# Optimization experiments

Hardware: AMD Instinct MI355X
Metric: run time of the kernel (lower is better)

## Reference

```python
import jax, jax.numpy as jnp
import numpy as np
from jax import lax

TOP_K = 8

B, S, D, N, R = 32, 128, 512, 131072, 16


def setup_inputs() -> dict:
    key = jax.random.key(0)
    ks = jax.random.split(key, 10)
    return {
        "query": jax.random.normal(ks[0], (B, S, D), jnp.float32),
        "base_memory": jax.random.normal(ks[1], (N, D), jnp.float32) * 0.01,
        "lora_A": jax.random.normal(ks[2], (N, R), jnp.float32) * 0.01,
        "lora_B": jax.random.normal(ks[3], (R, D), jnp.float32) * 0.01,
        "gru_w_ih": jax.random.normal(ks[4], (3 * D, D), jnp.float32) * 0.02,
        "gru_w_hh": jax.random.normal(ks[5], (3 * D, D), jnp.float32) * 0.02,
        "gru_b_ih": jax.random.normal(ks[6], (3 * D,), jnp.float32) * 0.02,
        "gru_b_hh": jax.random.normal(ks[7], (3 * D,), jnpp.float32) if False else jax.random.normal(ks[7], (3 * D,), jnp.float32) * 0.02,
        "wg_w": jax.random.normal(ks[8], (1, D), jnp.float32) * 0.02,
        "wg_b": jnp.zeros((1,), jnp.float32),
    }


def gru_cell(x, h, w_ih, w_hh, b_ih, b_hh):
    # torch.nn.GRUCell math; gates ordered [r, z, n]
    gx = x @ w_ih.T + b_ih            # [B, 3D]
    gh = h @ w_hh.T + b_hh            # [B, 3D]
    gx_r, gx_z, gx_n = jnp.split(gx, 3, axis=-1)
    gh_r, gh_z, gh_n = jnp.split(gh, 3, axis=-1)
    r = jax.nn.sigmoid(gx_r + gh_r)
    z = jax.nn.sigmoid(gx_z + gh_z)
    n = jnp.tanh(gx_n + r * gh_n)
    return (1.0 - z) * n + z * h


def reference(query, base_memory, lora_A, lora_B, gru_w_ih, gru_w_hh, gru_b_ih, gru_b_hh, wg_w, wg_b):
    mem = base_memory + lora_A @ lora_B                 # [N, D]
    q = query.mean(axis=1)                              # [B, D]
    scores = q @ mem.T                                  # [B, N]
    top_scores, top_idx = lax.top_k(scores, TOP_K)      # [B, K]
    retrieved = mem[top_idx]                            # [B, K, D] gather

    h0 = jnp.zeros_like(q)
    hidden = gru_cell(retrieved.sum(axis=1), h0, gru_w_ih, gru_w_hh, gru_b_ih, gru_b_hh)

    write_prob = jax.nn.sigmoid(hidden @ wg_w.T + wg_b)  # [B, 1]
    value = q                                            # value[b, 0] in torch == q[b]

    # Sequential over batch (matches torch loop order); within a batch the
    # top-k indices are distinct so a vectorized scatter-set is exact.
    def step(m, inp):
        idx, p, v = inp                                  # [K], scalar, [D]
        rows = (1.0 - p) * m[idx] + p * v
        return m.at[idx].set(rows), None

    new_mem, _ = lax.scan(step, base_memory, (top_idx, write_prob[:, 0], value))
    return retrieved, hidden, new_mem
```

## Files before the change

### kernel.cpp

```cpp
#include <hip/hip_runtime.h>
#include <math.h>

#define NROWS 131072
#define DDIM  512
#define BB    32
#define SS    128
#define KK    8

__global__ __launch_bounds__(256) void k_qmean(const float* __restrict__ query,
                                               float* __restrict__ q,
                                               float* __restrict__ pwsum) {
  __shared__ float part[256];
  int b  = blockIdx.x >> 3;
  int dc = blockIdx.x & 7;
  int t  = threadIdx.x;
  if (blockIdx.x == 0 && t < 32) pwsum[t] = 0.f;
  int lane = t & 63;
  int p    = t >> 6;
  const float* src = query + (size_t)b * SS * DDIM + (size_t)(p * 32) * DDIM
                   + dc * 64 + lane;
  float s = 0.f;
  #pragma unroll 8
  for (int i = 0; i < 32; ++i) s += src[(size_t)i * DDIM];
  part[t] = s;
  __syncthreads();
  if (t < 64) {
    float tot = part[t] + part[64 + t] + part[128 + t] + part[192 + t];
    q[b * DDIM + dc * 64 + t] = tot * (1.0f / 128.0f);
  }
}

__global__ __launch_bounds__(256) void k_mem(const float* __restrict__ base,
                                             const float* __restrict__ A,
                                             const float* __restrict__ Bm,
                                             float* __restrict__ newmem) {
  int gt = blockIdx.x * 256 + threadIdx.x;
  int c = gt & 127;
  int stream = gt >> 7;
  int row0 = stream * 64;
  int srow0 = __builtin_amdgcn_readfirstlane(row0);

  float4 Breg[16];
  #pragma unroll
  for (int r = 0; r < 16; ++r)
    Breg[r] = *(const float4*)(Bm + r * DDIM + 4 * c);

  const float* bp = base   + (size_t)row0 * DDIM + 4 * c;
  float*       np = newmem + (size_t)row0 * DDIM + 4 * c;

  float4 nxt0 = *(const float4*)(bp);
  float4 nxt1 = *(const float4*)(bp + DDIM);
  float4 nxt2 = *(const float4*)(bp + 2 * DDIM);
  float4 nxt3 = *(const float4*)(bp + 3 * DDIM);

  for (int i = 0; i < 64; i += 4) {
    float4 cur0 = nxt0, cur1 = nxt1, cur2 = nxt2, cur3 = nxt3;
    if (i + 4 < 64) {
      const float* p = bp + (size_t)(i + 4) * DDIM;
      nxt0 = *(const float4*)(p);
      nxt1 = *(const float4*)(p + DDIM);
      nxt2 = *(const float4*)(p + 2 * DDIM);
      nxt3 = *(const float4*)(p + 3 * DDIM);
    }
    #pragma unroll
    for (int k = 0; k < 4; ++k) {
      const float* Ar = A + (size_t)(srow0 + i + k) * 16;
      float4 acc = (k == 0) ? cur0 : (k == 1) ? cur1 : (k == 2) ? cur2 : cur3;
      #pragma unroll
      for (int r = 0; r < 16; ++r) {
        float a = Ar[r];
        acc.x += a * Breg[r].x; acc.y += a * Breg[r].y;
        acc.z += a * Breg[r].z; acc.w += a * Breg[r].w;
      }
      *(float4*)(np + (size_t)(i + k) * DDIM) = acc;
    }
  }
}

__global__ __launch_bounds__(256) void k_scores(const float* __restrict__ mem,
                                                const float* __restrict__ q,
                                                float* __restrict__ scores) {
  __shared__ float4 sq[4096];
  int t = threadIdx.x;
  const float4* qg = (const float4*)q;
  #pragma unroll
  for (int u = 0; u < 16; ++u) sq[u * 256 + t] = qg[u * 256 + t];
  __syncthreads();

  int r0 = blockIdx.x * 512 + t;
  float acc0[32], acc1[32];
  #pragma unroll
  for (int b = 0; b < 32; ++b) { acc0[b] = 0.f; acc1[b] = 0.f; }

  const float4* m0 = (const float4*)(mem + (size_t)r0 * DDIM);
  const float4* m1 = (const float4*)(mem + (size_t)(r0 + 256) * DDIM);

  float4 a_nxt0 = m0[0], a_nxt1 = m0[1], a_nxt2 = m0[2], a_nxt3 = m0[3];
  float4 b_nxt0 = m1[0], b_nxt1 = m1[1], b_nxt2 = m1[2], b_nxt3 = m1[3];

  for (int g = 0; g < 32; ++g) {
    float4 a0 = a_nxt0, a1 = a_nxt1, a2 = a_nxt2, a3 = a_nxt3;
    float4 c0 = b_nxt0, c1 = b_nxt1, c2 = b_nxt2, c3 = b_nxt3;
    if (g < 31) {
      int nb = 4 * (g + 1);
      a_nxt0 = m0[nb];     a_nxt1 = m0[nb + 1];
      a_nxt2 = m0[nb + 2]; a_nxt3 = m0[nb + 3];
      b_nxt0 = m1[nb];     b_nxt1 = m1[nb + 1];
      b_nxt2 = m1[nb + 2]; b_nxt3 = m1[nb + 3];
    }
    #pragma unroll
    for (int j = 0; j < 4; ++j) {
      int d4 = 4 * g + j;
      float4 x0 = (j == 0) ? a0 : (j == 1) ? a1 : (j == 2) ? a2 : a3;
      float4 x1 = (j == 0) ? c0 : (j == 1) ? c1 : (j == 2) ? c2 : c3;
      #pragma unroll
      for (int b = 0; b < 32; ++b) {
        float4 qv = sq[b * 128 + d4];
        acc0[b] += qv.x*x0.x + qv.y*x0.y + qv.z*x0.z + qv.w*x0.w;
        acc1[b] += qv.x*x1.x + qv.y*x1.y + qv.z*x1.z + qv.w*x1.w;
      }
    }
  }
  #pragma unroll
  for (int b = 0; b < 32; ++b) {
    scores[(size_t)b * NROWS + r0]       = acc0[b];
    scores[(size_t)b * NROWS + r0 + 256] = acc1[b];
  }
}

__device__ __forceinline__ void insert8(float (&v)[8], int (&ix)[8], float x, int i) {
  bool better = (x > v[7]) || (x == v[7] && i < ix[7]);
  if (!better) return;
  v[7] = x; ix[7] = i;
  #pragma unroll
  for (int u = 7; u > 0; --u) {
    bool sw = (v[u] > v[u-1]) || (v[u] == v[u-1] && ix[u] < ix[u-1]);
    if (sw) {
      float tv = v[u]; v[u] = v[u-1]; v[u-1] = tv;
      int ti = ix[u]; ix[u] = ix[u-1]; ix[u-1] = ti;
    }
  }
}

__global__ __launch_bounds__(256) void k_topk1(const float* __restrict__ scores,
                                               float* __restrict__ cval,
                                               int* __restrict__ cidx) {
  __shared__ float lval[256][8]; __shared__ int lidx[256][8];
  __shared__ float mval[32][8];  __shared__ int midx[32][8];
  int b = blockIdx.x >> 4, j = blockIdx.x & 15, t = threadIdx.x;
  const float4* s4 = (const float4*)(scores + (size_t)b * NROWS + j * 8192);

  float v[8]; int ix[8];
  #pragma unroll
  for (int e = 0; e < 8; ++e) { v[e] = -1e30f; ix[e] = 0x7fffffff; }
  #pragma unroll
  for (int i = 0; i < 8; ++i) {
    int f4 = i * 256 + t;
    float4 x = s4[f4];
    int n0 = j * 8192 + f4 * 4;
    insert8(v, ix, x.x, n0);
    insert8(v, ix, x.y, n0 + 1);
    insert8(v, ix, x.z, n0 + 2);
    insert8(v, ix, x.w, n0 + 3);
  }
  #pragma unroll
  for (int e = 0; e < 8; ++e) { lval[t][e] = v[e]; lidx[t][e] = ix[e]; }
  __syncthreads();

  if (t < 32) {
    float mv[8]; int mi[8];
    #pragma unroll
    for (int e = 0; e < 8; ++e) { mv[e] = -1e30f; mi[e] = 0x7fffffff; }
    for (int u = 0; u < 8; ++u) {
      int src = t * 8 + u;
      #pragma unroll
      for (int e = 0; e < 8; ++e) insert8(mv, mi, lval[src][e], lidx[src][e]);
    }
    #pragma unroll
    for (int e = 0; e < 8; ++e) { mval[t][e] = mv[e]; midx[t][e] = mi[e]; }
  }
  __syncthreads();

  if (t == 0) {
    float mv[8]; int mi[8];
    #pragma unroll
    for (int e = 0; e < 8; ++e) { mv[e] = -1e30f; mi[e] = 0x7fffffff; }
    for (int u = 0; u < 32; ++u)
      #pragma unroll
      for (int e = 0; e < 8; ++e) insert8(mv, mi, mval[u][e], midx[u][e]);
    #pragma unroll
    for (int e = 0; e < 8; ++e) {
      cval[(b * 16 + j) * 8 + e] = mv[e];
      cidx[(b * 16 + j) * 8 + e] = mi[e];
    }
  }
}

__global__ __launch_bounds__(128) void k_gather(const float* __restrict__ mem,
                                                const float* __restrict__ cval,
                                                const int* __restrict__ cidx,
                                                int* __restrict__ topidx,
                                                float* __restrict__ retrieved,
                                                float* __restrict__ x) {
  __shared__ float scv[128]; __shared__ int sci[128];
  __shared__ int stop[8];
  int b = blockIdx.x, t = threadIdx.x;
  scv[t] = cval[b * 128 + t];
  sci[t] = cidx[b * 128 + t];
  __syncthreads();
  if (t == 0) {
    float mv[8]; int mi[8];
    #pragma unroll
    for (int e = 0; e < 8; ++e) { mv[e] = -1e30f; mi[e] = 0x7fffffff; }
    for (int u = 0; u < 128; ++u) insert8(mv, mi, scv[u], sci[u]);
    #pragma unroll
    for (int e = 0; e < 8; ++e) { stop[e] = mi[e]; topidx[b * 8 + e] = mi[e]; }
  }
  __syncthreads();

  float4 xs = make_float4(0.f, 0.f, 0.f, 0.f);
  #pragma unroll
  for (int k = 0; k < 8; ++k) {
    int row = stop[k];
    float4 vv = *(const float4*)(mem + (size_t)row * DDIM + 4 * t);
    *(float4*)(retrieved + (size_t)(b * 8 + k) * DDIM + 4 * t) = vv;
    xs.x += vv.x; xs.y += vv.y; xs.z += vv.z; xs.w += vv.w;
  }
  *(float4*)(x + (size_t)b * DDIM + 4 * t) = xs;
}

__global__ __launch_bounds__(64) void k_gru(const float* __restrict__ x,
                                            const float* __restrict__ wih,
                                            const float* __restrict__ bih,
                                            const float* __restrict__ bhh,
                                            const float* __restrict__ wgw,
                                            float* __restrict__ hidden,
                                            float* __restrict__ pwsum) {
  int b     = blockIdx.x >> 3;
  int chunk = blockIdx.x & 7;
  int t = chunk * 64 + threadIdx.x;
  const float* xb = x + b * 512;
  const float* wr = wih + (size_t)t * 512;
  const float* wz = wih + (size_t)(512 + t) * 512;
  const float* wn = wih + (size_t)(1024 + t) * 512;
  float gr = 0.f, gz = 0.f, gn = 0.f;
  #pragma unroll 4
  for (int d4 = 0; d4 < 128; ++d4) {
    float4 xv = *(const float4*)(xb + 4 * d4);
    float4 a = *(const float4*)(wr + 4 * d4);
    float4 c = *(const float4*)(wz + 4 * d4);
    float4 e = *(const float4*)(wn + 4 * d4);
    gr += a.x*xv.x + a.y*xv.y + a.z*xv.z + a.w*xv.w;
    gz += c.x*xv.x + c.y*xv.y + c.z*xv.z + c.w*xv.w;
    gn += e.x*xv.x + e.y*xv.y + e.z*xv.z + e.w*xv.w;
  }
  float r = 1.f / (1.f + expf(-(gr + bih[t]        + bhh[t])));
  float z = 1.f / (1.f + expf(-(gz + bih[512 + t]  + bhh[512 + t])));
  float n = tanhf(gn + bih[1024 + t] + r * bhh[1024 + t]);
  float h = (1.f - z) * n;
  hidden[b * 512 + t] = h;

  float pw = h * wgw[t];
  #pragma unroll
  for (int off = 32; off > 0; off >>= 1) pw += __shfl_down(pw, off, 64);
  if (threadIdx.x == 0) atomicAdd(pwsum + b, pw);
}

__global__ __launch_bounds__(256) void k_scatter(float* __restrict__ newmem,
                                                 const int* __restrict__ topidx,
                                                 const float* __restrict__ pwsum,
                                                 const float* __restrict__ wgb,
                                                 const float* __restrict__ q) {
  int t = threadIdx.x;
  int d = blockIdx.x * 64 + (t & 63);
  int k0 = t >> 6;
  for (int b = 0; b < 32; ++b) {
    float p = 1.f / (1.f + expf(-(pwsum[b] + wgb[0])));
    float qv = q[b * 512 + d];
    #pragma unroll
    for (int kk = 0; kk < 2; ++kk) {
      int k = k0 + kk * 4;
      int row = topidx[b * 8 + k];
      size_t off = (size_t)row * 512 + d;
      float m = __hip_atomic_load(newmem + off, __ATOMIC_RELAXED,
                                  __HIP_MEMORY_SCOPE_AGENT);
      __hip_atomic_store(newmem + off, (1.f - p) * m + p * qv,
                         __ATOMIC_RELAXED, __HIP_MEMORY_SCOPE_AGENT);
    }
    __syncthreads();
  }
}

extern "C" void kernel_launch(void* const* d_in, const int* in_sizes, int n_in,
                              void* d_out, int out_size, void* d_ws, size_t ws_size,
                              hipStream_t stream) {
  const float* query = (const float*)d_in[0];
  const float* base  = (const float*)d_in[1];
  const float* lA    = (const float*)d_in[2];
  const float* lB    = (const float*)d_in[3];
  const float* wih   = (const float*)d_in[4];
  const float* bih   = (const float*)d_in[6];
  const float* bhh   = (const float*)d_in[7];
  const float* wgw   = (const float*)d_in[8];
  const float* wgb   = (const float*)d_in[9];

  float* out = (float*)d_out;
  float* retrieved = out;
  float* hidden    = out + 131072;
  float* newmem    = out + 147456;

  float* wq  = (float*)d_ws;
  float* wsc = wq + 16384;
  float* wx  = wsc + 4194304;
  float* wp  = wx + 16384;
  int*   wti = (int*)(wp + 32);
  float* wcv = (float*)(wti + 256);
  int*   wci = (int*)(wcv + 4096);

  k_qmean  <<<256,  256, 0, stream>>>(query, wq, wp);
  k_mem    <<<1024, 256, 0, stream>>>(base, lA, lB, newmem);
  k_scores <<<256,  256, 0, stream>>>(newmem, wq, wsc);
  k_topk1  <<<512,  256, 0, stream>>>(wsc, wcv, wci);
  k_gather <<<32,   128, 0, stream>>>(newmem, wcv, wci, wti, retrieved, wx);
  k_gru    <<<256,  64,  0, stream>>>(wx, wih, bih, bhh, wgw, hidden, wp);
  k_scatter<<<8,    256, 0, stream>>>(newmem, wti, wp, wgb, wq);
}
```

Measured before the change: 881.7 us.

## Transpose query means and stream them from global memory in the scores kernel

k_qmean now also writes a transposed copy of the mean queries (d-major, 32 batch values per dimension). k_scores drops the 64KB shared-memory staging of q and instead loads q columns for each d as uniform float4 reads, double-buffered in registers, with one memory row per thread and twice as many blocks. The aim is to remove LDS traffic and the large shared allocation that limited occupancy, and to halve per-thread accumulator registers so more waves can hide memory latency. The risk is that the uniform q loads go through scalar or vector cache every step and could become the bottleneck instead of LDS.

```diff
diff --git a/kernel.cpp b/kernel.cpp
--- a/kernel.cpp
+++ b/kernel.cpp
@@ -9,6 +9,7 @@
 
 __global__ __launch_bounds__(256) void k_qmean(const float* __restrict__ query,
                                                float* __restrict__ q,
+                                               float* __restrict__ qT,
                                                float* __restrict__ pwsum) {
   __shared__ float part[256];
   int b  = blockIdx.x >> 3;
@@ -26,7 +27,10 @@
   __syncthreads();
   if (t < 64) {
     float tot = part[t] + part[64 + t] + part[128 + t] + part[192 + t];
-    q[b * DDIM + dc * 64 + t] = tot * (1.0f / 128.0f);
+    float val = tot * (1.0f / 128.0f);
+    int d = dc * 64 + t;
+    q[b * DDIM + d]  = val;
+    qT[d * 32 + b]   = val;
   }
 }
 
@@ -78,54 +82,63 @@
 }
 
 __global__ __launch_bounds__(256) void k_scores(const float* __restrict__ mem,
-                                                const float* __restrict__ q,
+                                                const float* __restrict__ qT,
                                                 float* __restrict__ scores) {
-  __shared__ float4 sq[4096];
   int t = threadIdx.x;
-  const float4* qg = (const float4*)q;
-  #pragma unroll
-  for (int u = 0; u < 16; ++u) sq[u * 256 + t] = qg[u * 256 + t];
-  __syncthreads();
-
-  int r0 = blockIdx.x * 512 + t;
-  float acc0[32], acc1[32];
-  #pragma unroll
-  for (int b = 0; b < 32; ++b) { acc0[b] = 0.f; acc1[b] = 0.f; }
-
-  const float4* m0 = (const float4*)(mem + (size_t)r0 * DDIM);
-  const float4* m1 = (const float4*)(mem + (size_t)(r0 + 256) * DDIM);
-
-  float4 a_nxt0 = m0[0], a_nxt1 = m0[1], a_nxt2 = m0[2], a_nxt3 = m0[3];
-  float4 b_nxt0 = m1[0], b_nxt1 = m1[1], b_nxt2 = m1[2], b_nxt3 = m1[3];
+  int r = blockIdx.x * 256 + t;
+  float acc[32];
+  #pragma unroll
+  for (int b = 0; b < 32; ++b) acc[b] = 0.f;
+  const float4* mrow = (const float4*)(mem + (size_t)r * DDIM);
+
+  float4 qA[8], qB[8];
+  #pragma unroll
+  for (int u = 0; u < 8; ++u) qA[u] = *(const float4*)(qT + 4 * u);
+
+  float4 nxt0 = mrow[0], nxt1 = mrow[1], nxt2 = mrow[2], nxt3 = mrow[3];
 
   for (int g = 0; g < 32; ++g) {
-    float4 a0 = a_nxt0, a1 = a_nxt1, a2 = a_nxt2, a3 = a_nxt3;
-    float4 c0 = b_nxt0, c1 = b_nxt1, c2 = b_nxt2, c3 = b_nxt3;
+    float4 c0 = nxt0, c1 = nxt1, c2 = nxt2, c3 = nxt3;
     if (g < 31) {
-      int nb = 4 * (g + 1);
-      a_nxt0 = m0[nb];     a_nxt1 = m0[nb + 1];
-      a_nxt2 = m0[nb + 2]; a_nxt3 = m0[nb + 3];
-      b_nxt0 = m1[nb];     b_nxt1 = m1[nb + 1];
-      b_nxt2 = m1[nb + 2]; b_nxt3 = m1[nb + 3];
+      nxt0 = mrow[4 * g + 4]; nxt1 = mrow[4 * g + 5];
+      nxt2 = mrow[4 * g + 6]; nxt3 = mrow[4 * g + 7];
     }
     #pragma unroll
     for (int j = 0; j < 4; ++j) {
-      int d4 = 4 * g + j;
-      float4 x0 = (j == 0) ? a0 : (j == 1) ? a1 : (j == 2) ? a2 : a3;
-      float4 x1 = (j == 0) ? c0 : (j == 1) ? c1 : (j == 2) ? c2 : c3;
+      float4 mv = (j == 0) ? c0 : (j == 1) ? c1 : (j == 2) ? c2 : c3;
       #pragma unroll
-      for (int b = 0; b < 32; ++b) {
-        float4 qv = sq[b * 128 + d4];
-        acc0[b] += qv.x*x0.x + qv.y*x0.y + qv.z*x0.z + qv.w*x0.w;
-        acc1[b] += qv.x*x1.x + qv.y*x1.y + qv.z*x1.z + qv.w*x1.w;
+      for (int p = 0; p < 4; ++p) {
+        int d  = 16 * g + 4 * j + p;
+        int dn = (d + 1) & 511;
+        float mval = (p == 0) ? mv.x : (p == 1) ? mv.y : (p == 2) ? mv.z : mv.w;
+        if ((p & 1) == 0) {
+          #pragma unroll
+          for (int u = 0; u < 8; ++u)
+            qB[u] = *(const float4*)(qT + dn * 32 + 4 * u);
+          #pragma unroll
+          for (int b4 = 0; b4 < 8; ++b4) {
+            acc[4*b4+0] += qA[b4].x * mval;
+            acc[4*b4+1] += qA[b4].y * mval;
+            acc[4*b4+2] += qA[b4].z * mval;
+            acc[4*b4+3] += qA[b4].w * mval;
+          }
+        } else {
+          #pragma unroll
+          for (int u = 0; u < 8; ++u)
+            qA[u] = *(const float4*)(qT + dn * 32 + 4 * u);
+          #pragma unroll
+          for (int b4 = 0; b4 < 8; ++b4) {
+            acc[4*b4+0] += qB[b4].x * mval;
+            acc[4*b4+1] += qB[b4].y * mval;
+            acc[4*b4+2] += qB[b4].z * mval;
+            acc[4*b4+3] += qB[b4].w * mval;
+          }
+        }
       }
     }
   }
   #pragma unroll
-  for (int b = 0; b < 32; ++b) {
-    scores[(size_t)b * NROWS + r0]       = acc0[b];
-    scores[(size_t)b * NROWS + r0 + 256] = acc1[b];
-  }
+  for (int b = 0; b < 32; ++b) scores[(size_t)b * NROWS + r] = acc[b];
 }
 
 __device__ __forceinline__ void insert8(float (&v)[8], int (&ix)[8], float x, int i) {
@@ -310,16 +323,17 @@
   float* newmem    = out + 147456;
 
   float* wq  = (float*)d_ws;
-  float* wsc = wq + 16384;
+  float* wqT = wq + 16384;
+  float* wsc = wqT + 16384;
   float* wx  = wsc + 4194304;
   float* wp  = wx + 16384;
   int*   wti = (int*)(wp + 32);
   float* wcv = (float*)(wti + 256);
   int*   wci = (int*)(wcv + 4096);
 
-  k_qmean  <<<256,  256, 0, stream>>>(query, wq, wp);
+  k_qmean  <<<256,  256, 0, stream>>>(query, wq, wqT, wp);
   k_mem    <<<1024, 256, 0, stream>>>(base, lA, lB, newmem);
-  k_scores <<<256,  256, 0, stream>>>(newmem, wq, wsc);
+  k_scores <<<512,  256, 0, stream>>>(newmem, wqT, wsc);
   k_topk1  <<<512,  256, 0, stream>>>(wsc, wcv, wci);
   k_gather <<<32,   128, 0, stream>>>(newmem, wcv, wci, wti, retrieved, wx);
   k_gru    <<<256,  64,  0, stream>>>(wx, wih, bih, bhh, wgw, hidden, wp);
```

Result: faster. 822.3 us (-6.7%).
